# Optimization experiments

Hardware: AMD Instinct MI355X
Metric: run time of the kernel (lower is better)

Reference implementation:

```python
import jax, jax.numpy as jnp
import numpy as np

B, S, D = 4, 4096, 2048  # batch, seq, hidden
E, R, K = 8, 16, 2       # n_experts, rank, top_k


def setup_inputs() -> dict:
    key = jax.random.key(0)
    k1, k2, k3, k4 = jax.random.split(key, 4)
    x = jax.random.normal(k1, (B, S, D), dtype=jnp.float32)
    router_w = jax.random.normal(k2, (E, D), dtype=jnp.float32) * 0.02  # nn.Linear weight (out,in)
    experts_down = jax.random.normal(k3, (E, D, R), dtype=jnp.float32) * 0.01
    experts_up = jax.random.normal(k4, (E, R, D), dtype=jnp.float32) * 0.01
    return {"x": x, "router_w": router_w, "experts_down": experts_down, "experts_up": experts_up}


def reference(x, router_w, experts_down, experts_up):
    E_ = router_w.shape[0]
    # router sees detached x (torch: self.router(x.detach()))
    logits = jnp.einsum('bsd,ed->bse', jax.lax.stop_gradient(x), router_w)
    w, idx = jax.lax.top_k(logits, K)          # (B,S,K)
    w = jax.nn.softmax(w, axis=-1)
    # combined per-token, per-expert routing weight; zero for non-selected experts
    w_full = jnp.sum(jax.nn.one_hot(idx, E_, dtype=x.dtype) * w[..., None], axis=2)  # (B,S,E)
    # rank-space activations per expert: (B,S,E,R) -- small (R=16)
    h = jnp.einsum('bsd,edr->bser', x, experts_down)
    # fuse routing weight into rank space, then up-project and sum over experts
    out = x + jnp.einsum('bser,bse,erd->bsd', h, w_full, experts_up)
    return out
```

## Files before the change

kernel.cpp:

```cpp
#include <hip/hip_runtime.h>
#include <hip/hip_bf16.h>

#define MTOK 16384
#define DDIM 2048
#define NEXP 8
#define RNK 16
#define NC 128
#define NW 160
#define LOGIT0 128
#define KSPLIT 2
#define KLEN (DDIM / KSPLIT)
#define NT (KLEN / 64)

typedef __attribute__((ext_vector_type(8))) short bf16x8;
typedef __attribute__((ext_vector_type(4))) short short4v;
typedef __attribute__((ext_vector_type(4))) float f32x4;

typedef __attribute__((address_space(1))) const void gv_t;
typedef __attribute__((address_space(3))) void lv_t;

__device__ __forceinline__ short f2b(float f) {
  unsigned u = __float_as_uint(f);
  u += 0x7fffu + ((u >> 16) & 1u);
  return (short)(u >> 16);
}
__device__ __forceinline__ float b2f(short s) {
  return __uint_as_float(((unsigned)(unsigned short)s) << 16);
}

__global__ __launch_bounds__(256) void prep_k(const float* __restrict__ rw,
                                              const float* __restrict__ down,
                                              const float* __restrict__ up,
                                              short* __restrict__ WdT,
                                              short* __restrict__ UT) {
  int i = blockIdx.x * 256 + threadIdx.x;
  const int NWD = NW * DDIM;
  const int NUT = DDIM * NC;
  if (i < NWD) {
    int n = i / DDIM, k = i % DDIM;
    int s = (k >> 3) & 7;
    int src_k = (k & ~0x3F) | ((s ^ (n & 7)) << 3) | (k & 7);
    float v = 0.f;
    if (n < NC)             v = down[((n >> 4) * DDIM + src_k) * RNK + (n & 15)];
    else if (n < NC + NEXP) v = rw[(n - NC) * DDIM + src_k];
    WdT[i] = f2b(v);
  } else if (i < NWD + NUT) {
    int u = i - NWD;
    int d = u >> 7, c = u & 127;
    UT[u] = f2b(up[((c >> 4) * RNK + (c & 15)) * DDIM + d]);
  }
}

__global__ __launch_bounds__(256, 4) void gemm1_k(const float* __restrict__ X,
                                                  const short* __restrict__ WdT,
                                                  short* __restrict__ Hp) {
  __shared__ short Al[2][64][72];
  __shared__ short Bl[2][160 * 64];
  const int tid = threadIdx.x;
  const int lane = tid & 63;
  const int w = tid >> 6;
  const int gm0 = blockIdx.x * 64;
  const int ks = blockIdx.y;
  const int kb = ks * KLEN;
  const int wr = (w & 1) * 32;
  const int wc = (w >> 1) * 80;
  const int lr = lane & 15;
  const int lk = (lane >> 4) * 8;

  f32x4 acc[2][5];
#pragma unroll
  for (int m = 0; m < 2; ++m)
#pragma unroll
    for (int n = 0; n < 5; ++n) acc[m][n] = (f32x4){0.f, 0.f, 0.f, 0.f};

  float4 aR[2][4];

  auto loadA = [&](int k0, int s) {
#pragma unroll
    for (int i2 = 0; i2 < 4; ++i2) {
      int f = tid + 256 * i2;
      int row = f >> 4, c4 = f & 15;
      aR[s][i2] = *(const float4*)(X + (size_t)(gm0 + row) * DDIM + k0 + c4 * 4);
    }
  };
  auto issueB = [&](int buf, int k0) {
#pragma unroll
    for (int j = 0; j < 5; ++j) {
      int u = (w * 5 + j) * 64 + lane;
      const short* g = WdT + (size_t)(u >> 3) * DDIM + k0 + (u & 7) * 8;
      short* l = &Bl[buf][(w * 5 + j) * 512];
      __builtin_amdgcn_global_load_lds((gv_t*)g, (lv_t*)l, 16, 0, 0);
    }
  };
  auto writeA = [&](int buf, int s) {
#pragma unroll
    for (int i2 = 0; i2 < 4; ++i2) {
      int f = tid + 256 * i2;
      int row = f >> 4, c4 = f & 15;
      short4v v;
      v.x = f2b(aR[s][i2].x); v.y = f2b(aR[s][i2].y);
      v.z = f2b(aR[s][i2].z); v.w = f2b(aR[s][i2].w);
      *(short4v*)&Al[buf][row][c4 * 4] = v;
    }
  };
  auto compute = [&](int buf) {
#pragma unroll
    for (int kk2 = 0; kk2 < 2; ++kk2) {
      const int kk = kk2 * 32;
      bf16x8 a[2], b[5];
#pragma unroll
      for (int m = 0; m < 2; ++m)
        a[m] = *(const bf16x8*)&Al[buf][wr + m * 16 + lr][kk + lk];
#pragma unroll
      for (int n = 0; n < 5; ++n) {
        int row = wc + n * 16 + lr;
        int sl = ((kk >> 3) + (lane >> 4)) ^ (row & 7);
        b[n] = *(const bf16x8*)&Bl[buf][row * 64 + sl * 8];
      }
#pragma unroll
      for (int m = 0; m < 2; ++m)
#pragma unroll
        for (int n = 0; n < 5; ++n)
          acc[m][n] = __builtin_amdgcn_mfma_f32_16x16x32_bf16(a[m], b[n], acc[m][n], 0, 0, 0);
    }
  };

  loadA(kb, 0);
  issueB(0, kb);
  loadA(kb + 64, 1);
  issueB(1, kb + 64);
  asm volatile("s_waitcnt vmcnt(12)" ::: "memory");
  __builtin_amdgcn_sched_barrier(0);
  writeA(0, 0);
  asm volatile("s_waitcnt vmcnt(7)" ::: "memory");
  asm volatile("s_waitcnt lgkmcnt(0)" ::: "memory");
  __builtin_amdgcn_sched_barrier(0);
  __builtin_amdgcn_s_barrier();

#pragma unroll
  for (int t = 0; t < NT; ++t) {
    if (t + 2 < NT) loadA(kb + (t + 2) * 64, t & 1);
    compute(t & 1);
    asm volatile("s_waitcnt lgkmcnt(0)" ::: "memory");
    __builtin_amdgcn_s_barrier();
    __builtin_amdgcn_sched_barrier(0);
    if (t + 2 < NT) issueB(t & 1, kb + (t + 2) * 64);
    if (t + 1 < NT) {
      if (t + 2 < NT)
        asm volatile("s_waitcnt vmcnt(7)" ::: "memory");
      else
        asm volatile("s_waitcnt vmcnt(0)" ::: "memory");
      __builtin_amdgcn_sched_barrier(0);
      writeA((t + 1) & 1, (t + 1) & 1);
      asm volatile("s_waitcnt lgkmcnt(0)" ::: "memory");
      __builtin_amdgcn_sched_barrier(0);
    }
    __builtin_amdgcn_s_barrier();
  }

  short* Hq = Hp + (size_t)ks * MTOK * NW;
  const int cr = (lane >> 4) * 4;
#pragma unroll
  for (int m = 0; m < 2; ++m)
#pragma unroll
    for (int n = 0; n < 5; ++n)
#pragma unroll
      for (int r = 0; r < 4; ++r) {
        int row = gm0 + wr + m * 16 + cr + r;
        int col = wc + n * 16 + lr;
        Hq[(size_t)row * NW + col] = f2b(acc[m][n][r]);
      }
}

__global__ __launch_bounds__(256) void route_k(const short* __restrict__ Hp,
                                               short* __restrict__ Hw) {
  __shared__ float wv[64][8];
  const int tid = threadIdx.x;
  const int t0 = blockIdx.x * 64;
  const short* H0 = Hp;
  const short* H1 = Hp + (size_t)MTOK * NW;
  if (tid < 64) {
    int t = t0 + tid;
    uint4 l0 = *(const uint4*)(H0 + (size_t)t * NW + LOGIT0);
    uint4 l1 = *(const uint4*)(H1 + (size_t)t * NW + LOGIT0);
    const short* p0 = (const short*)&l0;
    const short* p1 = (const short*)&l1;
    float b0 = -1e30f, b1 = -1e30f;
    int i0 = 0, i1 = 0;
#pragma unroll
    for (int e = 0; e < 8; ++e) {
      float v = b2f(p0[e]) + b2f(p1[e]);
      if (v > b0) { b1 = b0; i1 = i0; b0 = v; i0 = e; }
      else if (v > b1) { b1 = v; i1 = e; }
    }
    float ex = __expf(b1 - b0);
    float inv = 1.f / (1.f + ex);
#pragma unroll
    for (int e = 0; e < 8; ++e)
      wv[tid][e] = (e == i0) ? inv : ((e == i1) ? ex * inv : 0.f);
  }
  __syncthreads();
  const int t = tid >> 2, q = tid & 3;
  const short* a0 = H0 + (size_t)(t0 + t) * NW + q * 32;
  const short* a1 = H1 + (size_t)(t0 + t) * NW + q * 32;
  short* o = Hw + (size_t)(t0 + t) * NC + q * 32;
#pragma unroll
  for (int j = 0; j < 4; ++j) {
    uint4 v0 = *(const uint4*)(a0 + j * 8);
    uint4 v1 = *(const uint4*)(a1 + j * 8);
    const short* s0 = (const short*)&v0;
    const short* s1 = (const short*)&v1;
    short r[8];
    int cbase = q * 32 + j * 8;
#pragma unroll
    for (int e2 = 0; e2 < 8; ++e2) {
      float h = b2f(s0[e2]) + b2f(s1[e2]);
      r[e2] = f2b(h * wv[t][(cbase + e2) >> 4]);
    }
    *(uint4*)(o + j * 8) = *(uint4*)r;
  }
}

__global__ __launch_bounds__(256) void gemm2_k(const short* __restrict__ Hw,
                                               const short* __restrict__ UT,
                                               const float* __restrict__ X,
                                               float* __restrict__ Out) {
  __shared__ short Al[128][136];
  __shared__ short Bl[64][136];
  const int tid = threadIdx.x;
  const int lane = tid & 63;
  const int w = tid >> 6;
  const int gm0 = blockIdx.x * 128;
  const int n0 = blockIdx.y * 64;
  const int lr = lane & 15;
  const int lk = (lane >> 4) * 8;

#pragma unroll
  for (int i = 0; i < 8; ++i) {
    int f = tid + 256 * i;
    int row = f >> 4, c8 = f & 15;
    *(uint4*)&Al[row][c8 * 8] = *(const uint4*)(Hw + (size_t)(gm0 + row) * NC + c8 * 8);
  }
#pragma unroll
  for (int i = 0; i < 4; ++i) {
    int f = tid + 256 * i;
    int row = f >> 4, c8 = f & 15;
    *(uint4*)&Bl[row][c8 * 8] = *(const uint4*)(UT + (size_t)(n0 + row) * NC + c8 * 8);
  }
  __syncthreads();

  f32x4 acc[2][4];
#pragma unroll
  for (int m = 0; m < 2; ++m)
#pragma unroll
    for (int n = 0; n < 4; ++n) acc[m][n] = (f32x4){0.f, 0.f, 0.f, 0.f};

#pragma unroll
  for (int ks = 0; ks < 4; ++ks) {
    const int kk = ks * 32;
    bf16x8 a[2], b[4];
#pragma unroll
    for (int m = 0; m < 2; ++m) a[m] = *(const bf16x8*)&Al[w * 32 + m * 16 + lr][kk + lk];
#pragma unroll
    for (int n = 0; n < 4; ++n) b[n] = *(const bf16x8*)&Bl[n * 16 + lr][kk + lk];
#pragma unroll
    for (int m = 0; m < 2; ++m)
#pragma unroll
      for (int n = 0; n < 4; ++n)
        acc[m][n] = __builtin_amdgcn_mfma_f32_16x16x32_bf16(a[m], b[n], acc[m][n], 0, 0, 0);
  }

  float* eps = (float*)&Al[0][0] + w * 2176;
  const int cr = (lane >> 4) * 4;
#pragma unroll
  for (int m = 0; m < 2; ++m)
#pragma unroll
    for (int n = 0; n < 4; ++n)
#pragma unroll
      for (int r = 0; r < 4; ++r)
        eps[(m * 16 + cr + r) * 68 + n * 16 + lr] = acc[m][n][r];

#pragma unroll
  for (int j = 0; j < 8; ++j) {
    int c = lane + 64 * j;
    int rl = c >> 4, c4 = c & 15;
    float4 v = *(const float4*)&eps[rl * 68 + c4 * 4];
    size_t idx = (size_t)(gm0 + w * 32 + rl) * DDIM + n0 + c4 * 4;
    const float4 xv = *(const float4*)(X + idx);
    v.x += xv.x; v.y += xv.y; v.z += xv.z; v.w += xv.w;
    *(float4*)(Out + idx) = v;
  }
}

extern "C" void kernel_launch(void* const* d_in, const int* in_sizes, int n_in,
                              void* d_out, int out_size, void* d_ws, size_t ws_size,
                              hipStream_t stream) {
  const float* x    = (const float*)d_in[0];
  const float* rw   = (const float*)d_in[1];
  const float* down = (const float*)d_in[2];
  const float* up   = (const float*)d_in[3];
  float* out = (float*)d_out;

  char* ws = (char*)d_ws;
  short* WdT = (short*)ws;
  short* UT  = (short*)(ws + 655360);
  short* Hp  = (short*)(ws + 1179648);
  short* Hw  = (short*)(ws + 11665408);

  prep_k<<<2304, 256, 0, stream>>>(rw, down, up, WdT, UT);
  gemm1_k<<<dim3(MTOK / 64, KSPLIT), 256, 0, stream>>>(x, WdT, Hp);
  route_k<<<MTOK / 64, 256, 0, stream>>>(Hp, Hw);
  gemm2_k<<<dim3(MTOK / 128, DDIM / 64), 256, 0, stream>>>(Hw, UT, x, out);
}
```

Baseline: 87.00 us.

## Fuse routing and split-K reduction into gemm2 and prefetch residual

Removes the separate route_k kernel. gemm2 now computes the top-2 softmax weights per token and sums the two split-K partials while it stages the rank-space tile into shared memory. The residual X tile is also prefetched into registers before the staging step, so its load latency overlaps with the other work. This saves one launch and the Hw round trip through global memory. The cost is that the routing and partial-sum work is repeated in each of the 32 column blocks, and the prefetch adds register pressure.

```diff
diff --git a/kernel.cpp b/kernel.cpp
--- a/kernel.cpp
+++ b/kernel.cpp
@@ -46,8 +46,8 @@
     WdT[i] = f2b(v);
   } else if (i < NWD + NUT) {
     int u = i - NWD;
-    int d = u >> 7, c = u & 127;
-    UT[u] = f2b(up[((c >> 4) * RNK + (c & 15)) * DDIM + d]);
+    int c = u >> 7, j = u & 127;
+    UT[u] = f2b(up[((j >> 4) * RNK + (j & 15)) * DDIM + c]);
   }
 }
 
@@ -172,56 +172,7 @@
       }
 }
 
-__global__ __launch_bounds__(256) void route_k(const short* __restrict__ Hp,
-                                               short* __restrict__ Hw) {
-  __shared__ float wv[64][8];
-  const int tid = threadIdx.x;
-  const int t0 = blockIdx.x * 64;
-  const short* H0 = Hp;
-  const short* H1 = Hp + (size_t)MTOK * NW;
-  if (tid < 64) {
-    int t = t0 + tid;
-    uint4 l0 = *(const uint4*)(H0 + (size_t)t * NW + LOGIT0);
-    uint4 l1 = *(const uint4*)(H1 + (size_t)t * NW + LOGIT0);
-    const short* p0 = (const short*)&l0;
-    const short* p1 = (const short*)&l1;
-    float b0 = -1e30f, b1 = -1e30f;
-    int i0 = 0, i1 = 0;
-#pragma unroll
-    for (int e = 0; e < 8; ++e) {
-      float v = b2f(p0[e]) + b2f(p1[e]);
-      if (v > b0) { b1 = b0; i1 = i0; b0 = v; i0 = e; }
-      else if (v > b1) { b1 = v; i1 = e; }
-    }
-    float ex = __expf(b1 - b0);
-    float inv = 1.f / (1.f + ex);
-#pragma unroll
-    for (int e = 0; e < 8; ++e)
-      wv[tid][e] = (e == i0) ? inv : ((e == i1) ? ex * inv : 0.f);
-  }
-  __syncthreads();
-  const int t = tid >> 2, q = tid & 3;
-  const short* a0 = H0 + (size_t)(t0 + t) * NW + q * 32;
-  const short* a1 = H1 + (size_t)(t0 + t) * NW + q * 32;
-  short* o = Hw + (size_t)(t0 + t) * NC + q * 32;
-#pragma unroll
-  for (int j = 0; j < 4; ++j) {
-    uint4 v0 = *(const uint4*)(a0 + j * 8);
-    uint4 v1 = *(const uint4*)(a1 + j * 8);
-    const short* s0 = (const short*)&v0;
-    const short* s1 = (const short*)&v1;
-    short r[8];
-    int cbase = q * 32 + j * 8;
-#pragma unroll
-    for (int e2 = 0; e2 < 8; ++e2) {
-      float h = b2f(s0[e2]) + b2f(s1[e2]);
-      r[e2] = f2b(h * wv[t][(cbase + e2) >> 4]);
-    }
-    *(uint4*)(o + j * 8) = *(uint4*)r;
-  }
-}
-
-__global__ __launch_bounds__(256) void gemm2_k(const short* __restrict__ Hw,
+__global__ __launch_bounds__(256) void gemm2_k(const short* __restrict__ Hp,
                                                const short* __restrict__ UT,
                                                const float* __restrict__ X,
                                                float* __restrict__ Out) {
@@ -234,18 +185,61 @@
   const int n0 = blockIdx.y * 64;
   const int lr = lane & 15;
   const int lk = (lane >> 4) * 8;
-
-#pragma unroll
-  for (int i = 0; i < 8; ++i) {
-    int f = tid + 256 * i;
-    int row = f >> 4, c8 = f & 15;
-    *(uint4*)&Al[row][c8 * 8] = *(const uint4*)(Hw + (size_t)(gm0 + row) * NC + c8 * 8);
+  const short* Hp1 = Hp + (size_t)MTOK * NW;
+
+  float4 xPf[8];
+#pragma unroll
+  for (int j = 0; j < 8; ++j) {
+    int c = lane + 64 * j;
+    int rl = c >> 4, c4 = c & 15;
+    xPf[j] = *(const float4*)(X + (size_t)(gm0 + w * 32 + rl) * DDIM + n0 + c4 * 4);
+  }
+
+  if (tid < 128) {
+    int t = gm0 + tid;
+    uint4 l0 = *(const uint4*)(Hp  + (size_t)t * NW + LOGIT0);
+    uint4 l1 = *(const uint4*)(Hp1 + (size_t)t * NW + LOGIT0);
+    const short* p0 = (const short*)&l0;
+    const short* p1 = (const short*)&l1;
+    float lgv[8];
+#pragma unroll
+    for (int e = 0; e < 8; ++e) lgv[e] = b2f(p0[e]) + b2f(p1[e]);
+    float b0 = -1e30f, b1 = -1e30f;
+    int i0 = 0, i1 = 0;
+#pragma unroll
+    for (int e = 0; e < 8; ++e) {
+      float v = lgv[e];
+      if (v > b0) { b1 = b0; i1 = i0; b0 = v; i0 = e; }
+      else if (v > b1) { b1 = v; i1 = e; }
+    }
+    float ex = __expf(b1 - b0);
+    float inv = 1.f / (1.f + ex);
+#pragma unroll
+    for (int e = 0; e < 8; ++e)
+      Al[tid][128 + e] = f2b((e == i0) ? inv : ((e == i1) ? ex * inv : 0.f));
   }
 #pragma unroll
   for (int i = 0; i < 4; ++i) {
     int f = tid + 256 * i;
     int row = f >> 4, c8 = f & 15;
     *(uint4*)&Bl[row][c8 * 8] = *(const uint4*)(UT + (size_t)(n0 + row) * NC + c8 * 8);
+  }
+  __syncthreads();
+
+#pragma unroll
+  for (int i = 0; i < 8; ++i) {
+    int f = tid + 256 * i;
+    int row = f >> 4, c8 = f & 15;
+    uint4 h0 = *(const uint4*)(Hp  + (size_t)(gm0 + row) * NW + c8 * 8);
+    uint4 h1 = *(const uint4*)(Hp1 + (size_t)(gm0 + row) * NW + c8 * 8);
+    const short* p0 = (const short*)&h0;
+    const short* p1 = (const short*)&h1;
+    float wgt = b2f(Al[row][128 + (c8 >> 1)]);
+    short r[8];
+#pragma unroll
+    for (int e = 0; e < 8; ++e)
+      r[e] = f2b((b2f(p0[e]) + b2f(p1[e])) * wgt);
+    *(uint4*)&Al[row][c8 * 8] = *(uint4*)r;
   }
   __syncthreads();
 
@@ -286,8 +280,7 @@
     int rl = c >> 4, c4 = c & 15;
     float4 v = *(const float4*)&eps[rl * 68 + c4 * 4];
     size_t idx = (size_t)(gm0 + w * 32 + rl) * DDIM + n0 + c4 * 4;
-    const float4 xv = *(const float4*)(X + idx);
-    v.x += xv.x; v.y += xv.y; v.z += xv.z; v.w += xv.w;
+    v.x += xPf[j].x; v.y += xPf[j].y; v.z += xPf[j].z; v.w += xPf[j].w;
     *(float4*)(Out + idx) = v;
   }
 }
@@ -305,10 +298,8 @@
   short* WdT = (short*)ws;
   short* UT  = (short*)(ws + 655360);
   short* Hp  = (short*)(ws + 1179648);
-  short* Hw  = (short*)(ws + 11665408);
 
   prep_k<<<2304, 256, 0, stream>>>(rw, down, up, WdT, UT);
   gemm1_k<<<dim3(MTOK / 64, KSPLIT), 256, 0, stream>>>(x, WdT, Hp);
-  route_k<<<MTOK / 64, 256, 0, stream>>>(Hp, Hw);
-  gemm2_k<<<dim3(MTOK / 128, DDIM / 64), 256, 0, stream>>>(Hw, UT, x, out);
-}
+  gemm2_k<<<dim3(MTOK / 128, DDIM / 64), 256, 0, stream>>>(Hp, UT, x, out);
+}
```

Result: slower. 92.07 us (+5.8%).
